# Kernel tuning notes

Measured on AMD Instinct MI355X. Metric: run time of the kernel, lower is better.

The kernel has to match this reference:

```python
import jax, jax.numpy as jnp
import numpy as np
import math

WIN = 8
N = WIN * WIN          # window_area = 64
H = 6                  # num_heads
DH = 32                # head_dim = dim // num_heads
DIM = 192
B_ = 8192              # batch * num_windows
LOG_MAX = math.log(1.0 / 0.01)
EPS = 1e-12            # F.normalize eps


def _checkerboard_mask():
    wm = np.ones((WIN, WIN))
    wm[0::2, 1::2] = 0
    wm[1::2, 0::2] = 0
    f = wm.reshape(-1)
    return jnp.asarray(np.outer(f, f).astype(bool))  # [N, N], True = keep


def _rel_pos_index():
    coords = np.stack(np.meshgrid(np.arange(WIN), np.arange(WIN), indexing='ij'))
    cf = coords.reshape(2, -1)
    rel = (cf[:, :, None] - cf[:, None, :]).transpose(1, 2, 0).copy()
    rel[:, :, 0] += WIN - 1
    rel[:, :, 1] += WIN - 1
    rel[:, :, 0] *= 2 * WIN - 1
    return rel.sum(-1).astype(np.int32)  # [N, N] in [0, 224]


def setup_inputs() -> dict:
    key = jax.random.key(0)
    ks = jax.random.split(key, 5)
    return {
        'x': jax.random.normal(ks[0], (B_, N, DIM), jnp.float32),
        'qkv_w': jax.random.normal(ks[1], (3 * H * DH, DIM), jnp.float32) * 0.02,
        'qkv_b': jnp.zeros((3 * H * DH,), jnp.float32),
        'proj_w': jax.random.normal(ks[2], (DIM, H * DH), jnp.float32) * 0.02,
        'proj_b': jnp.zeros((DIM,), jnp.float32),
        'logit_scale': jnp.full((H, 1, 1), math.log(10.0), jnp.float32),
        'rel_bias_table': jax.random.normal(ks[3], ((2 * WIN - 1) ** 2, H), jnp.float32) * 0.02,
        'rel_pos_index': jnp.asarray(_rel_pos_index()),
    }


def _l2norm(t):
    n = jnp.linalg.norm(t, axis=-1, keepdims=True)
    return t / jnp.maximum(n, EPS)


def reference(x, qkv_w, qkv_b, proj_w, proj_b, logit_scale, rel_bias_table, rel_pos_index):
    B = x.shape[0]
    # qkv projection -> [3, B, H, N, DH]
    qkv = (jnp.einsum('bnc,oc->bno', x, qkv_w) + qkv_b)
    qkv = qkv.reshape(B, N, 3, H, DH).transpose(2, 0, 3, 1, 4)
    q, k, v = qkv[0], qkv[1], qkv[2]

    # cosine-similarity attention logits
    attn = jnp.einsum('bhnd,bhmd->bhnm', _l2norm(q), _l2norm(k))
    scale = jnp.exp(jnp.minimum(logit_scale, LOG_MAX))  # [H,1,1]
    attn = attn * scale[None]

    # relative position bias: gather [N*N,H] -> [1,H,N,N]
    bias = rel_bias_table[rel_pos_index.reshape(-1)].reshape(N, N, H).transpose(2, 0, 1)
    attn = attn + bias[None]

    # checkerboard mask + softmax with fully-masked-row (NaN) fixup -> zeros
    cb = _checkerboard_mask()[None, None]  # [1,1,N,N]
    neg = jnp.where(cb, attn, -jnp.inf)
    m = jnp.max(neg, axis=-1, keepdims=True)
    m_safe = jnp.where(jnp.isfinite(m), m, 0.0)
    e = jnp.where(cb, jnp.exp(neg - m_safe), 0.0)
    s = jnp.sum(e, axis=-1, keepdims=True)
    p = jnp.where(s > 0, e / jnp.where(s > 0, s, 1.0), 0.0)

    out = jnp.einsum('bhnm,bhmd->bhnd', p, v)
    out = out.transpose(0, 2, 1, 3).reshape(B, N, H * DH)
    return jnp.einsum('bnd,od->bno', out, proj_w) + proj_b
```

## Files before the change

### kernel.cpp

```cpp
#include <hip/hip_runtime.h>

typedef _Float16 h8 __attribute__((ext_vector_type(8)));
typedef _Float16 h2 __attribute__((ext_vector_type(2)));
typedef float f4 __attribute__((ext_vector_type(4)));

#define NHEADS 6
#define LOGMAX 4.6051701859880914f
#define LOG2E  1.4426950408889634f

__device__ __forceinline__ int S_of(int j) { return ((j >> 2) << 3) + ((j & 3) << 1) + ((j >> 2) & 1); }
__device__ __forceinline__ int SC_of(int j) { return ((j >> 2) << 3) + ((j & 3) << 1) + (1 - ((j >> 2) & 1)); }

template <int CTRL>
__device__ __forceinline__ float dpp_mov(float x) {
    return __builtin_bit_cast(float,
        __builtin_amdgcn_update_dpp(0, __builtin_bit_cast(int, x), CTRL, 0xF, 0xF, true));
}
__device__ __forceinline__ float rowsum16(float x) {
    x += dpp_mov<0x121>(x);
    x += dpp_mov<0x122>(x);
    x += dpp_mov<0x124>(x);
    x += dpp_mov<0x128>(x);
    return x;
}
__device__ __forceinline__ unsigned pack2(float a, float b) {
    h2 v; v[0] = (_Float16)a; v[1] = (_Float16)b;
    return __builtin_bit_cast(unsigned, v);
}
__device__ __forceinline__ float fast_exp2(float x) {
    float r; asm("v_exp_f32 %0, %1" : "=v"(r) : "v"(x)); return r;
}
__device__ __forceinline__ float fast_rcp(float x) {
    float r; asm("v_rcp_f32 %0, %1" : "=v"(r) : "v"(x)); return r;
}
__device__ __forceinline__ float fast_rsq(float x) {
    float r; asm("v_rsq_f32 %0, %1" : "=v"(r) : "v"(x)); return r;
}

__global__ void pack_kernel(const float* __restrict__ qkv_w,
                            const float* __restrict__ proj_w,
                            const float* __restrict__ rel_bias_table,
                            const int* __restrict__ rel_pos_index,
                            const float* __restrict__ logit_scale,
                            _Float16* __restrict__ qkvp,
                            _Float16* __restrict__ projp,
                            float* __restrict__ b2t,
                            float* __restrict__ sl2t) {
    int tid = blockIdx.x * 256 + threadIdx.x;
    const int NQ = 6 * 6 * 6 * 64;
    const int NP = 6 * 12 * 64;
    if (tid < NQ) {
        int l = tid & 63;
        int rest = tid >> 6;
        int ks = rest % 6;
        int nt = (rest / 6) % 6;
        int h = rest / 36;
        int o = (nt >> 1) * 192 + h * 32 + (nt & 1) * 16 + (l & 15);
        int k0 = ks * 32 + (l >> 4) * 8;
        const float* src = qkv_w + o * 192 + k0;
        _Float16* dst = qkvp + tid * 8;
#pragma unroll
        for (int j = 0; j < 8; ++j) dst[j] = (_Float16)src[j];
    } else if (tid < NQ + NP) {
        int t = tid - NQ;
        int l = t & 63;
        int rest = t >> 6;
        int nt = rest % 12;
        int h = rest / 12;
        int o = nt * 16 + (l & 15);
        const float* srcrow = proj_w + o * 192 + h * 32;
        _Float16* dst = projp + t * 8;
        int p0 = (l >> 4) * 8;
#pragma unroll
        for (int j = 0; j < 8; ++j) {
            int p = p0 + j;
            dst[j] = (_Float16)srcrow[(p >> 1) + ((p & 1) << 4)];
        }
    } else if (tid < NQ + NP + 6 * 32 * 32) {
        int t = tid - (NQ + NP);
        int h = t >> 10;
        int jr = (t >> 5) & 31;
        int ic = t & 31;
        int rp = rel_pos_index[S_of(jr) * 64 + S_of(ic)];
        float scale = __expf(fminf(logit_scale[h], LOGMAX));
        b2t[t] = (rel_bias_table[rp * NHEADS + h] - scale - 1.0f) * LOG2E;
        if (jr == 0 && ic == 0) sl2t[h] = scale * LOG2E;
    }
}

__global__ __launch_bounds__(256) __attribute__((amdgpu_waves_per_eu(3, 8)))
void cwa_kernel(
    const float* __restrict__ x,
    const _Float16* __restrict__ qkvp,
    const _Float16* __restrict__ projp,
    const float* __restrict__ b2t,
    const float* __restrict__ sl2t,
    const float* __restrict__ qkv_b,
    const float* __restrict__ proj_b,
    float* __restrict__ out) {
    __shared__ __align__(16) _Float16 wbuf[6 * 6 * 64 * 8];
    __shared__ __align__(16) unsigned knu[2][32][20];
    __shared__ __align__(16) _Float16 vT[2][32][40];
    __shared__ __align__(16) unsigned tmpu[4][16][20];

    const int tid = threadIdx.x;
    const int lane = tid & 63;
    const int wave = tid >> 6;
    const int cl = lane & 15;
    const int g = lane >> 4;
    const int w0 = blockIdx.x * 2;
    const int w = wave >> 1;
    const int mh = wave & 1;

    auto stage = [&](int h) {
        const _Float16* srcb = qkvp + (long)h * (6 * 6 * 64 * 8) + (wave * 9) * 512 + lane * 8;
        _Float16* dstb = &wbuf[(wave * 9) * 512];
#pragma unroll
        for (int c = 0; c < 9; ++c)
            __builtin_amdgcn_global_load_lds(
                (const __attribute__((address_space(1))) unsigned*)(srcb + c * 512),
                (__attribute__((address_space(3))) unsigned*)(dstb + c * 512),
                16, 0, 0);
    };

    stage(0);

    {
        int rowi = tid >> 2;
        int sub = tid & 3;
        long base = ((long)(w0 + (rowi >> 5)) * 64 + SC_of(rowi & 31)) * 192;
#pragma unroll
        for (int i = 0; i < 12; ++i) {
            int c4 = i * 4 + sub;
            *(f4*)(out + base + c4 * 4) = *(const f4*)(proj_b + c4 * 4);
        }
    }

    h8 xf[6];
    {
        long xbase = ((long)(w0 + w) * 64 + S_of(mh * 16 + cl)) * 192;
#pragma unroll
        for (int ks = 0; ks < 6; ++ks) {
            f4 u0 = *(const f4*)(x + xbase + ks * 32 + g * 8);
            f4 u1 = *(const f4*)(x + xbase + ks * 32 + g * 8 + 4);
            h8 hv;
            hv[0] = (_Float16)u0[0]; hv[1] = (_Float16)u0[1];
            hv[2] = (_Float16)u0[2]; hv[3] = (_Float16)u0[3];
            hv[4] = (_Float16)u1[0]; hv[5] = (_Float16)u1[1];
            hv[6] = (_Float16)u1[2]; hv[7] = (_Float16)u1[3];
            xf[ks] = hv;
        }
    }

    f4 pacc[12];
#pragma unroll
    for (int nt = 0; nt < 12; ++nt) pacc[nt] = 0.0f;

#pragma unroll 1
    for (int h = 0; h < NHEADS; ++h) {
        asm volatile("s_waitcnt vmcnt(0)" ::: "memory");
        __builtin_amdgcn_s_barrier();

        f4 acc[6];
#pragma unroll
        for (int nt = 0; nt < 6; ++nt) acc[nt] = 0.0f;
#pragma unroll
        for (int ks = 0; ks < 6; ++ks) {
#pragma unroll
            for (int nt = 0; nt < 6; ++nt) {
                h8 b = *(const h8*)(&wbuf[((nt * 6 + ks) * 64 + lane) * 8]);
                acc[nt] = __builtin_amdgcn_mfma_f32_16x16x32_f16(xf[ks], b, acc[nt], 0, 0, 0);
            }
        }
        asm volatile("s_waitcnt lgkmcnt(0)" ::: "memory");
        __builtin_amdgcn_s_barrier();
        if (h + 1 < NHEADS) stage(h + 1);

        float bq0 = qkv_b[h * 32 + cl], bq1 = qkv_b[h * 32 + 16 + cl];
        float bk0 = qkv_b[192 + h * 32 + cl], bk1 = qkv_b[192 + h * 32 + 16 + cl];
        float bv0 = qkv_b[384 + h * 32 + cl], bv1 = qkv_b[384 + h * 32 + 16 + cl];
        unsigned qw[4], kw[4];
        float vv0[4], vv1[4];
#pragma unroll
        for (int r = 0; r < 4; ++r) {
            float t0 = acc[0][r] + bq0, t1 = acc[1][r] + bq1;
            float ss = rowsum16(fmaf(t0, t0, t1 * t1));
            float rs = fast_rsq(fmaxf(ss, 1e-24f));
            qw[r] = pack2(t0 * rs, t1 * rs);
            t0 = acc[2][r] + bk0; t1 = acc[3][r] + bk1;
            ss = rowsum16(fmaf(t0, t0, t1 * t1));
            rs = fast_rsq(fmaxf(ss, 1e-24f));
            kw[r] = pack2(t0 * rs, t1 * rs);
            vv0[r] = acc[4][r] + bv0;
            vv1[r] = acc[5][r] + bv1;
        }
#pragma unroll
        for (int r = 0; r < 4; ++r) {
            int q = g * 4 + r;
            tmpu[wave][q][cl] = qw[r];
            knu[w][mh * 16 + q][cl] = kw[r];
            int kvpos = 2 * q + mh;
            vT[w][cl][kvpos] = (_Float16)vv0[r];
            vT[w][16 + cl][kvpos] = (_Float16)vv1[r];
        }
        asm volatile("s_waitcnt lgkmcnt(0)" ::: "memory");
        __builtin_amdgcn_s_barrier();

        {
            h8 aq = *(const h8*)(&tmpu[wave][cl][g * 4]);
            f4 sN[2];
            sN[0] = 0.0f; sN[1] = 0.0f;
#pragma unroll
            for (int nt = 0; nt < 2; ++nt) {
                h8 bk_ = *(const h8*)(&knu[w][nt * 16 + cl][g * 4]);
                sN[nt] = __builtin_amdgcn_mfma_f32_16x16x32_f16(aq, bk_, sN[nt], 0, 0, 0);
            }
            float sl2 = sl2t[h];
            const float* b2row = b2t + h * 1024 + (mh * 16 + g * 4) * 32;
            unsigned pw[4];
            float invr[4];
#pragma unroll
            for (int r = 0; r < 4; ++r) {
                float e0 = fast_exp2(fmaf(sN[0][r], sl2, b2row[r * 32 + cl]));
                float e1 = fast_exp2(fmaf(sN[1][r], sl2, b2row[r * 32 + 16 + cl]));
                invr[r] = rowsum16(e0 + e1);
                pw[r] = pack2(e0, e1);
            }
#pragma unroll
            for (int r = 0; r < 4; ++r) {
                invr[r] = fast_rcp(invr[r]);
                tmpu[wave][g * 4 + r][cl] = pw[r];
            }
            h8 ap = *(const h8*)(&tmpu[wave][cl][g * 4]);
            f4 ov[2];
            ov[0] = 0.0f; ov[1] = 0.0f;
#pragma unroll
            for (int nt = 0; nt < 2; ++nt) {
                h8 bv_ = *(const h8*)(&vT[w][nt * 16 + cl][g * 8]);
                ov[nt] = __builtin_amdgcn_mfma_f32_16x16x32_f16(ap, bv_, ov[nt], 0, 0, 0);
            }
#pragma unroll
            for (int r = 0; r < 4; ++r)
                tmpu[wave][g * 4 + r][cl] = pack2(ov[0][r] * invr[r], ov[1][r] * invr[r]);
            h8 am = *(const h8*)(&tmpu[wave][cl][g * 4]);
            const _Float16* pp_h = projp + (long)h * 12 * 64 * 8;
#pragma unroll
            for (int nt = 0; nt < 12; ++nt) {
                h8 bp = *(const h8*)(pp_h + ((nt * 64 + lane) << 3));
                pacc[nt] = __builtin_amdgcn_mfma_f32_16x16x32_f16(am, bp, pacc[nt], 0, 0, 0);
            }
        }
    }

#pragma unroll
    for (int r = 0; r < 4; ++r) {
        long grow = (long)(w0 + w) * 64 + S_of(mh * 16 + g * 4 + r);
        float* po_ = out + grow * 192 + cl;
#pragma unroll
        for (int nt = 0; nt < 12; ++nt)
            po_[nt * 16] = pacc[nt][r] + proj_b[nt * 16 + cl];
    }
}

extern "C" void kernel_launch(void* const* d_in, const int* in_sizes, int n_in,
                              void* d_out, int out_size, void* d_ws, size_t ws_size,
                              hipStream_t stream) {
    const float* x = (const float*)d_in[0];
    const float* qkv_w = (const float*)d_in[1];
    const float* qkv_b = (const float*)d_in[2];
    const float* proj_w = (const float*)d_in[3];
    const float* proj_b = (const float*)d_in[4];
    const float* logit_scale = (const float*)d_in[5];
    const float* rel_bias_table = (const float*)d_in[6];
    const int* rel_pos_index = (const int*)d_in[7];
    float* out = (float*)d_out;

    const int B = in_sizes[0] / (64 * 192);

    _Float16* qkvp = (_Float16*)d_ws;
    _Float16* projp = qkvp + 6 * 6 * 6 * 64 * 8;
    float* b2t = (float*)(projp + 6 * 12 * 64 * 8);
    float* sl2t = b2t + 6 * 32 * 32;

    pack_kernel<<<96, 256, 0, stream>>>(qkv_w, proj_w, rel_bias_table, rel_pos_index,
                                        logit_scale, qkvp, projp, b2t, sl2t);
    cwa_kernel<<<B / 2, 256, 0, stream>>>(x, qkvp, projp, b2t, sl2t, qkv_b, proj_b,
                                          out);
}
```

Baseline: 218.7 us.

## Give each wave a whole window to double weight reuse and drop barrier

Each wave now handles one full window (32 kept rows, two 16-row M tiles) instead of half a window. Each block covers four windows, so every weight fragment read from LDS and every proj weight load feeds two MFMAs. Because all K/V data for a window lives in one wave, the block barrier between the QKV epilogue and the attention step is removed. The cost is roughly double the accumulator registers, and occupancy is pinned to 2 waves per EU, which may hurt latency hiding.

```diff
diff --git a/kernel.cpp b/kernel.cpp
--- a/kernel.cpp
+++ b/kernel.cpp
@@ -88,7 +88,7 @@
     }
 }
 
-__global__ __launch_bounds__(256) __attribute__((amdgpu_waves_per_eu(3, 8)))
+__global__ __launch_bounds__(256) __attribute__((amdgpu_waves_per_eu(2, 2)))
 void cwa_kernel(
     const float* __restrict__ x,
     const _Float16* __restrict__ qkvp,
@@ -99,18 +99,17 @@
     const float* __restrict__ proj_b,
     float* __restrict__ out) {
     __shared__ __align__(16) _Float16 wbuf[6 * 6 * 64 * 8];
-    __shared__ __align__(16) unsigned knu[2][32][20];
-    __shared__ __align__(16) _Float16 vT[2][32][40];
-    __shared__ __align__(16) unsigned tmpu[4][16][20];
+    __shared__ __align__(16) unsigned knu[4][32][20];
+    __shared__ __align__(16) _Float16 vT[4][32][40];
+    __shared__ __align__(16) unsigned tmpu[4][32][20];
 
     const int tid = threadIdx.x;
     const int lane = tid & 63;
     const int wave = tid >> 6;
     const int cl = lane & 15;
     const int g = lane >> 4;
-    const int w0 = blockIdx.x * 2;
-    const int w = wave >> 1;
-    const int mh = wave & 1;
+    const long w0 = (long)blockIdx.x * 4;
+    const long win = w0 + wave;
 
     auto stage = [&](int h) {
         const _Float16* srcb = qkvp + (long)h * (6 * 6 * 64 * 8) + (wave * 9) * 512 + lane * 8;
@@ -125,20 +124,20 @@
 
     stage(0);
 
-    {
-        int rowi = tid >> 2;
-        int sub = tid & 3;
-        long base = ((long)(w0 + (rowi >> 5)) * 64 + SC_of(rowi & 31)) * 192;
-#pragma unroll
-        for (int i = 0; i < 12; ++i) {
-            int c4 = i * 4 + sub;
-            *(f4*)(out + base + c4 * 4) = *(const f4*)(proj_b + c4 * 4);
-        }
-    }
-
-    h8 xf[6];
-    {
-        long xbase = ((long)(w0 + w) * 64 + S_of(mh * 16 + cl)) * 192;
+#pragma unroll
+    for (int it = 0; it < 24; ++it) {
+        int e = tid + it * 256;
+        int wl = e / 1536;
+        int rem = e - wl * 1536;
+        int row = rem / 48, c4 = rem - row * 48;
+        *(f4*)(out + ((w0 + wl) * 64 + SC_of(row)) * 192 + c4 * 4) =
+            *(const f4*)(proj_b + c4 * 4);
+    }
+
+    h8 xf[2][6];
+#pragma unroll
+    for (int mt = 0; mt < 2; ++mt) {
+        long xbase = (win * 64 + S_of(mt * 16 + cl)) * 192;
 #pragma unroll
         for (int ks = 0; ks < 6; ++ks) {
             f4 u0 = *(const f4*)(x + xbase + ks * 32 + g * 8);
@@ -148,28 +147,33 @@
             hv[2] = (_Float16)u0[2]; hv[3] = (_Float16)u0[3];
             hv[4] = (_Float16)u1[0]; hv[5] = (_Float16)u1[1];
             hv[6] = (_Float16)u1[2]; hv[7] = (_Float16)u1[3];
-            xf[ks] = hv;
-        }
-    }
-
-    f4 pacc[12];
-#pragma unroll
-    for (int nt = 0; nt < 12; ++nt) pacc[nt] = 0.0f;
+            xf[mt][ks] = hv;
+        }
+    }
+
+    f4 pacc[2][12];
+#pragma unroll
+    for (int mt = 0; mt < 2; ++mt)
+#pragma unroll
+        for (int nt = 0; nt < 12; ++nt) pacc[mt][nt] = 0.0f;
 
 #pragma unroll 1
     for (int h = 0; h < NHEADS; ++h) {
         asm volatile("s_waitcnt vmcnt(0)" ::: "memory");
         __builtin_amdgcn_s_barrier();
 
-        f4 acc[6];
-#pragma unroll
-        for (int nt = 0; nt < 6; ++nt) acc[nt] = 0.0f;
+        f4 acc[2][6];
+#pragma unroll
+        for (int mt = 0; mt < 2; ++mt)
+#pragma unroll
+            for (int nt = 0; nt < 6; ++nt) acc[mt][nt] = 0.0f;
 #pragma unroll
         for (int ks = 0; ks < 6; ++ks) {
 #pragma unroll
             for (int nt = 0; nt < 6; ++nt) {
                 h8 b = *(const h8*)(&wbuf[((nt * 6 + ks) * 64 + lane) * 8]);
-                acc[nt] = __builtin_amdgcn_mfma_f32_16x16x32_f16(xf[ks], b, acc[nt], 0, 0, 0);
+                acc[0][nt] = __builtin_amdgcn_mfma_f32_16x16x32_f16(xf[0][ks], b, acc[0][nt], 0, 0, 0);
+                acc[1][nt] = __builtin_amdgcn_mfma_f32_16x16x32_f16(xf[1][ks], b, acc[1][nt], 0, 0, 0);
             }
         }
         asm volatile("s_waitcnt lgkmcnt(0)" ::: "memory");
@@ -179,87 +183,92 @@
         float bq0 = qkv_b[h * 32 + cl], bq1 = qkv_b[h * 32 + 16 + cl];
         float bk0 = qkv_b[192 + h * 32 + cl], bk1 = qkv_b[192 + h * 32 + 16 + cl];
         float bv0 = qkv_b[384 + h * 32 + cl], bv1 = qkv_b[384 + h * 32 + 16 + cl];
-        unsigned qw[4], kw[4];
-        float vv0[4], vv1[4];
-#pragma unroll
-        for (int r = 0; r < 4; ++r) {
-            float t0 = acc[0][r] + bq0, t1 = acc[1][r] + bq1;
-            float ss = rowsum16(fmaf(t0, t0, t1 * t1));
-            float rs = fast_rsq(fmaxf(ss, 1e-24f));
-            qw[r] = pack2(t0 * rs, t1 * rs);
-            t0 = acc[2][r] + bk0; t1 = acc[3][r] + bk1;
-            ss = rowsum16(fmaf(t0, t0, t1 * t1));
-            rs = fast_rsq(fmaxf(ss, 1e-24f));
-            kw[r] = pack2(t0 * rs, t1 * rs);
-            vv0[r] = acc[4][r] + bv0;
-            vv1[r] = acc[5][r] + bv1;
-        }
-#pragma unroll
-        for (int r = 0; r < 4; ++r) {
-            int q = g * 4 + r;
-            tmpu[wave][q][cl] = qw[r];
-            knu[w][mh * 16 + q][cl] = kw[r];
-            int kvpos = 2 * q + mh;
-            vT[w][cl][kvpos] = (_Float16)vv0[r];
-            vT[w][16 + cl][kvpos] = (_Float16)vv1[r];
-        }
-        asm volatile("s_waitcnt lgkmcnt(0)" ::: "memory");
-        __builtin_amdgcn_s_barrier();
+#pragma unroll
+        for (int mt = 0; mt < 2; ++mt)
+#pragma unroll
+            for (int r = 0; r < 4; ++r) {
+                int row = mt * 16 + g * 4 + r;
+                float t0 = acc[mt][0][r] + bq0, t1 = acc[mt][1][r] + bq1;
+                float ss = rowsum16(fmaf(t0, t0, t1 * t1));
+                float rs = fast_rsq(fmaxf(ss, 1e-24f));
+                tmpu[wave][row][cl] = pack2(t0 * rs, t1 * rs);
+                t0 = acc[mt][2][r] + bk0; t1 = acc[mt][3][r] + bk1;
+                ss = rowsum16(fmaf(t0, t0, t1 * t1));
+                rs = fast_rsq(fmaxf(ss, 1e-24f));
+                knu[wave][row][cl] = pack2(t0 * rs, t1 * rs);
+                int pos = 2 * (g * 4 + r) + mt;
+                vT[wave][cl][pos] = (_Float16)(acc[mt][4][r] + bv0);
+                vT[wave][16 + cl][pos] = (_Float16)(acc[mt][5][r] + bv1);
+            }
 
         {
-            h8 aq = *(const h8*)(&tmpu[wave][cl][g * 4]);
-            f4 sN[2];
-            sN[0] = 0.0f; sN[1] = 0.0f;
-#pragma unroll
-            for (int nt = 0; nt < 2; ++nt) {
-                h8 bk_ = *(const h8*)(&knu[w][nt * 16 + cl][g * 4]);
-                sN[nt] = __builtin_amdgcn_mfma_f32_16x16x32_f16(aq, bk_, sN[nt], 0, 0, 0);
-            }
+            h8 aq0 = *(const h8*)(&tmpu[wave][cl][g * 4]);
+            h8 aq1 = *(const h8*)(&tmpu[wave][16 + cl][g * 4]);
+            h8 bk0_ = *(const h8*)(&knu[wave][cl][g * 4]);
+            h8 bk1_ = *(const h8*)(&knu[wave][16 + cl][g * 4]);
+            f4 s[2][2];
+            s[0][0] = 0.0f; s[0][1] = 0.0f; s[1][0] = 0.0f; s[1][1] = 0.0f;
+            s[0][0] = __builtin_amdgcn_mfma_f32_16x16x32_f16(aq0, bk0_, s[0][0], 0, 0, 0);
+            s[0][1] = __builtin_amdgcn_mfma_f32_16x16x32_f16(aq0, bk1_, s[0][1], 0, 0, 0);
+            s[1][0] = __builtin_amdgcn_mfma_f32_16x16x32_f16(aq1, bk0_, s[1][0], 0, 0, 0);
+            s[1][1] = __builtin_amdgcn_mfma_f32_16x16x32_f16(aq1, bk1_, s[1][1], 0, 0, 0);
+
             float sl2 = sl2t[h];
-            const float* b2row = b2t + h * 1024 + (mh * 16 + g * 4) * 32;
-            unsigned pw[4];
-            float invr[4];
-#pragma unroll
-            for (int r = 0; r < 4; ++r) {
-                float e0 = fast_exp2(fmaf(sN[0][r], sl2, b2row[r * 32 + cl]));
-                float e1 = fast_exp2(fmaf(sN[1][r], sl2, b2row[r * 32 + 16 + cl]));
-                invr[r] = rowsum16(e0 + e1);
-                pw[r] = pack2(e0, e1);
-            }
-#pragma unroll
-            for (int r = 0; r < 4; ++r) {
-                invr[r] = fast_rcp(invr[r]);
-                tmpu[wave][g * 4 + r][cl] = pw[r];
-            }
-            h8 ap = *(const h8*)(&tmpu[wave][cl][g * 4]);
-            f4 ov[2];
-            ov[0] = 0.0f; ov[1] = 0.0f;
-#pragma unroll
-            for (int nt = 0; nt < 2; ++nt) {
-                h8 bv_ = *(const h8*)(&vT[w][nt * 16 + cl][g * 8]);
-                ov[nt] = __builtin_amdgcn_mfma_f32_16x16x32_f16(ap, bv_, ov[nt], 0, 0, 0);
-            }
-#pragma unroll
-            for (int r = 0; r < 4; ++r)
-                tmpu[wave][g * 4 + r][cl] = pack2(ov[0][r] * invr[r], ov[1][r] * invr[r]);
-            h8 am = *(const h8*)(&tmpu[wave][cl][g * 4]);
+            float invr[2][4];
+#pragma unroll
+            for (int mt = 0; mt < 2; ++mt)
+#pragma unroll
+                for (int r = 0; r < 4; ++r) {
+                    int row = mt * 16 + g * 4 + r;
+                    float e0 = fast_exp2(fmaf(s[mt][0][r], sl2, b2t[h * 1024 + row * 32 + cl]));
+                    float e1 = fast_exp2(fmaf(s[mt][1][r], sl2, b2t[h * 1024 + row * 32 + 16 + cl]));
+                    invr[mt][r] = rowsum16(e0 + e1);
+                    tmpu[wave][row][cl] = pack2(e0, e1);
+                }
+#pragma unroll
+            for (int mt = 0; mt < 2; ++mt)
+#pragma unroll
+                for (int r = 0; r < 4; ++r) invr[mt][r] = fast_rcp(invr[mt][r]);
+
+            h8 ap0 = *(const h8*)(&tmpu[wave][cl][g * 4]);
+            h8 ap1 = *(const h8*)(&tmpu[wave][16 + cl][g * 4]);
+            h8 bv0_ = *(const h8*)(&vT[wave][cl][g * 8]);
+            h8 bv1_ = *(const h8*)(&vT[wave][16 + cl][g * 8]);
+            f4 ov[2][2];
+            ov[0][0] = 0.0f; ov[0][1] = 0.0f; ov[1][0] = 0.0f; ov[1][1] = 0.0f;
+            ov[0][0] = __builtin_amdgcn_mfma_f32_16x16x32_f16(ap0, bv0_, ov[0][0], 0, 0, 0);
+            ov[0][1] = __builtin_amdgcn_mfma_f32_16x16x32_f16(ap0, bv1_, ov[0][1], 0, 0, 0);
+            ov[1][0] = __builtin_amdgcn_mfma_f32_16x16x32_f16(ap1, bv0_, ov[1][0], 0, 0, 0);
+            ov[1][1] = __builtin_amdgcn_mfma_f32_16x16x32_f16(ap1, bv1_, ov[1][1], 0, 0, 0);
+
+#pragma unroll
+            for (int mt = 0; mt < 2; ++mt)
+#pragma unroll
+                for (int r = 0; r < 4; ++r)
+                    tmpu[wave][mt * 16 + g * 4 + r][cl] =
+                        pack2(ov[mt][0][r] * invr[mt][r], ov[mt][1][r] * invr[mt][r]);
+            h8 am0 = *(const h8*)(&tmpu[wave][cl][g * 4]);
+            h8 am1 = *(const h8*)(&tmpu[wave][16 + cl][g * 4]);
             const _Float16* pp_h = projp + (long)h * 12 * 64 * 8;
 #pragma unroll
             for (int nt = 0; nt < 12; ++nt) {
                 h8 bp = *(const h8*)(pp_h + ((nt * 64 + lane) << 3));
-                pacc[nt] = __builtin_amdgcn_mfma_f32_16x16x32_f16(am, bp, pacc[nt], 0, 0, 0);
+                pacc[0][nt] = __builtin_amdgcn_mfma_f32_16x16x32_f16(am0, bp, pacc[0][nt], 0, 0, 0);
+                pacc[1][nt] = __builtin_amdgcn_mfma_f32_16x16x32_f16(am1, bp, pacc[1][nt], 0, 0, 0);
             }
         }
     }
 
 #pragma unroll
-    for (int r = 0; r < 4; ++r) {
-        long grow = (long)(w0 + w) * 64 + S_of(mh * 16 + g * 4 + r);
-        float* po_ = out + grow * 192 + cl;
-#pragma unroll
-        for (int nt = 0; nt < 12; ++nt)
-            po_[nt * 16] = pacc[nt][r] + proj_b[nt * 16 + cl];
-    }
+    for (int mt = 0; mt < 2; ++mt)
+#pragma unroll
+        for (int r = 0; r < 4; ++r) {
+            long grow = win * 64 + S_of(mt * 16 + g * 4 + r);
+            float* po_ = out + grow * 192 + cl;
+#pragma unroll
+            for (int nt = 0; nt < 12; ++nt)
+                po_[nt * 16] = pacc[mt][nt][r] + proj_b[nt * 16 + cl];
+        }
 }
 
 extern "C" void kernel_launch(void* const* d_in, const int* in_sizes, int n_in,
@@ -284,6 +293,6 @@
 
     pack_kernel<<<96, 256, 0, stream>>>(qkv_w, proj_w, rel_bias_table, rel_pos_index,
                                         logit_scale, qkvp, projp, b2t, sl2t);
-    cwa_kernel<<<B / 2, 256, 0, stream>>>(x, qkvp, projp, b2t, sl2t, qkv_b, proj_b,
+    cwa_kernel<<<B / 4, 256, 0, stream>>>(x, qkvp, projp, b2t, sl2t, qkv_b, proj_b,
                                           out);
 }
```

Result: no change. 218.2 us (-0.2%).
